# Kernel tuning notes

Measured on AMD Instinct MI355X. Metric: run time of the kernel, lower is better.

Reference implementation:

```python
import jax, jax.numpy as jnp
import numpy as np
import math

ATTN_C = 32
HEADS = 8
IN_C = 256
PAIR_C = 128
B, M, N = 1, 128, 256


def _layernorm(x, w, b, eps=1e-5):
    mu = jnp.mean(x, axis=-1, keepdims=True)
    xc = x - mu
    var = jnp.mean(xc * xc, axis=-1, keepdims=True)
    return xc * jax.lax.rsqrt(var + eps) * w + b


def setup_inputs() -> dict:
    key = jax.random.key(0)
    ks = jax.random.split(key, 10)
    s1 = 1.0 / math.sqrt(IN_C)
    s2 = 1.0 / math.sqrt(PAIR_C)
    s3 = 1.0 / math.sqrt(ATTN_C * HEADS)
    return {
        "x1d": jax.random.normal(ks[0], (B, M, N, IN_C), jnp.float32),
        "x2d": jax.random.normal(ks[1], (B, N, N, PAIR_C), jnp.float32),
        "norm_w": jnp.ones((IN_C,), jnp.float32),
        "norm_b": jnp.zeros((IN_C,), jnp.float32),
        "qkv_w": jax.random.normal(ks[2], (3 * ATTN_C * HEADS, IN_C), jnp.float32) * s1,
        "x2d_w": jax.random.normal(ks[3], (HEADS, PAIR_C), jnp.float32) * s2,
        "gate_w": jax.random.normal(ks[4], (ATTN_C * HEADS, IN_C), jnp.float32) * s1,
        "gate_b": jnp.zeros((ATTN_C * HEADS,), jnp.float32),
        "final_w": jax.random.normal(ks[5], (IN_C, ATTN_C * HEADS), jnp.float32) * s3,
        "final_b": jnp.zeros((IN_C,), jnp.float32),
    }


def reference(x1d, x2d, norm_w, norm_b, qkv_w, x2d_w, gate_w, gate_b, final_w, final_b):
    c, h = ATTN_C, HEADS
    x = _layernorm(x1d, norm_w, norm_b)                      # [B,M,N,IN_C]
    qkv = (x @ qkv_w.T).reshape(*x.shape[:-1], c, 3 * h)     # [B,M,N,c,3h]
    q, k, v = qkv[..., :h], qkv[..., h:2 * h], qkv[..., 2 * h:]
    aff = jnp.einsum('bmich,bmjch->bmijh', q, k)             # [B,M,N,N,H]
    gate = jax.nn.sigmoid(x @ gate_w.T + gate_b).reshape(*x.shape[:-1], c, h)
    factor = 1.0 / math.sqrt(c)
    bias = (x2d @ x2d_w.T) * factor                          # [B,N,N,H]
    weights = jax.nn.softmax(aff + bias[:, None], axis=-2)   # softmax over j
    out = jnp.einsum('bmrch,bmirh->bmich', v, weights) * gate
    out = out.reshape(*x.shape[:-1], c * h) @ final_w.T + final_b
    return out
```

## Files before the change

### kernel.cpp

```cpp
#include <hip/hip_runtime.h>
#include <math.h>

typedef short bf16x8 __attribute__((ext_vector_type(8)));
typedef float f32x4  __attribute__((ext_vector_type(4)));

#define NPOS 32768

#define OFF_CHI   0u
#define OFF_AHI   100663296u
#define OFF_ATTN  134217728u
#define OFF_BIAST 150994944u
#define OFF_WHI   153354240u
#define OFF_W2P   154402816u
#define OFF_GBP   154533888u

__device__ __forceinline__ short f2bf(float x) {
    unsigned int u = __float_as_uint(x);
    unsigned int r = (u + 0x7FFFu + ((u >> 16) & 1u)) >> 16;
    return (short)r;
}
__device__ __forceinline__ float bf2f(short s) {
    return __uint_as_float(((unsigned int)(unsigned short)s) << 16);
}
__device__ __forceinline__ void async_copy16(const void* g, void* l) {
    __builtin_amdgcn_global_load_lds(
        (const __attribute__((address_space(1))) unsigned int*)g,
        (__attribute__((address_space(3))) unsigned int*)l, 16, 0, 0);
}

#define PREP_LN   8192
#define PREP_CW   9473
__global__ __launch_bounds__(256) void k_prep(
    const float* __restrict__ x, const float* __restrict__ nw, const float* __restrict__ nb,
    const float* __restrict__ qkvw, const float* __restrict__ gatew,
    const float* __restrict__ gateb, const float* __restrict__ finalw,
    const float* __restrict__ x2d, const float* __restrict__ x2dw,
    short* __restrict__ Ahi, short* __restrict__ Whi, short* __restrict__ W2p,
    float* __restrict__ gbp, float* __restrict__ biasT) {
    __shared__ float xs[64][132];
    __shared__ float ws[8][132];
    const int bid = blockIdx.x;
    const int t = threadIdx.x;

    if (bid < PREP_LN) {
        int wid = (bid * 256 + t) >> 6;
        int lane = t & 63;
        const float4 v = ((const float4*)(x + (size_t)wid * 256))[lane];
        float s  = v.x + v.y + v.z + v.w;
        float ss = v.x*v.x + v.y*v.y + v.z*v.z + v.w*v.w;
        #pragma unroll
        for (int o = 32; o; o >>= 1) {
            s  += __shfl_xor(s,  o, 64);
            ss += __shfl_xor(ss, o, 64);
        }
        float mu  = s * (1.0f / 256);
        float var = ss * (1.0f / 256) - mu * mu;
        float rs  = rsqrtf(var + 1e-5f);
        const float4 wv = ((const float4*)nw)[lane];
        const float4 bv = ((const float4*)nb)[lane];
        float y[4] = {(v.x - mu) * rs * wv.x + bv.x, (v.y - mu) * rs * wv.y + bv.y,
                      (v.z - mu) * rs * wv.z + bv.z, (v.w - mu) * rs * wv.w + bv.w};
        short h4[4];
        #pragma unroll
        for (int i = 0; i < 4; ++i) h4[i] = f2bf(y[i]);
        *(short4*)(Ahi + (size_t)wid * 256 + lane * 4) = *(short4*)h4;
    } else if (bid < PREP_CW) {
        int r = bid - PREP_LN;
        if (r < 1024) {
            int which = r >> 8, h = (r >> 5) & 7, c = r & 31;
            const float* src = (which < 3) ? qkvw + (size_t)(c * 24 + which * 8 + h) * 256
                                           : gatew + (size_t)(c * 8 + h) * 256;
            Whi[(size_t)r * 256 + t] = f2bf(src[t]);
        } else if (r < 1280) {
            int o = r - 1024;
            int h = t >> 5, c = t & 31;
            W2p[(size_t)o * 256 + t] = f2bf(finalw[(size_t)o * 256 + c * 8 + h]);
        } else {
            int h = t >> 5, c = t & 31;
            gbp[t] = gateb[c * 8 + h];
        }
    } else {
        const int wid0 = (bid - PREP_CW) * 64;
        #pragma unroll
        for (int r = 0; r < 8; ++r) {
            int g = r * 256 + t;
            int row = g >> 5, c4 = g & 31;
            float4 v = *(const float4*)(x2d + (size_t)(wid0 + row) * 128 + c4 * 4);
            *(float4*)&xs[row][c4 * 4] = v;
        }
        {
            int h = t >> 5, c4 = t & 31;
            *(float4*)&ws[h][c4 * 4] = *(const float4*)(x2dw + h * 128 + c4 * 4);
        }
        __syncthreads();
        const float f = 0.17677669529663687f;
        const int i = wid0 >> 8;
        #pragma unroll
        for (int kk = 0; kk < 2; ++kk) {
            int o = t + kk * 256;
            int row = o >> 3, h = o & 7;
            float acc = 0.f;
            #pragma unroll
            for (int c4 = 0; c4 < 32; ++c4) {
                float4 xv = *(const float4*)&xs[row][c4 * 4];
                float4 wv = *(const float4*)&ws[h][c4 * 4];
                acc += xv.x * wv.x + xv.y * wv.y + xv.z * wv.z + xv.w * wv.w;
            }
            int j = (wid0 & 255) + row;
            biasT[(((h * 256 + j)) << 8) + i] = acc * f;
        }
    }
}

__global__ __launch_bounds__(256, 2) void k_gemm1m(
    const short* __restrict__ Ahi, const short* __restrict__ Whi,
    const float* __restrict__ gbp, short* __restrict__ Chi) {
    __shared__ short As[256 * 64];
    __shared__ short Bs[128 * 64];
    const int t = threadIdx.x;
    const int wave = t >> 6, lane = t & 63, ln15 = lane & 15, quad = lane >> 4;
    const int posBase = blockIdx.x * 256;
    const int nb = blockIdx.y;

    f32x4 acc[4][8];
    #pragma unroll
    for (int a = 0; a < 4; ++a)
        #pragma unroll
        for (int b = 0; b < 8; ++b) acc[a][b] = (f32x4){0.f, 0.f, 0.f, 0.f};

    for (int k0 = 0; k0 < 256; k0 += 64) {
        #pragma unroll
        for (int r = 0; r < 8; ++r) {
            int g = r * 256 + t;
            int row = g >> 3, cs = g & 7;
            int colg = cs ^ (row & 7);
            async_copy16(Ahi + (size_t)(posBase + row) * 256 + k0 + colg * 8, &As[g * 8]);
        }
        #pragma unroll
        for (int r = 0; r < 4; ++r) {
            int g = r * 256 + t;
            int row = g >> 3, cs = g & 7;
            int colg = cs ^ (row & 7);
            async_copy16(Whi + (size_t)(nb * 128 + row) * 256 + k0 + colg * 8, &Bs[g * 8]);
        }
        __syncthreads();
        #pragma unroll
        for (int kc = 0; kc < 2; ++kc) {
            bf16x8 af[4], bfr[8];
            #pragma unroll
            for (int it = 0; it < 4; ++it) {
                int rowa = wave * 64 + it * 16 + ln15;
                int c8a = (kc * 4 + quad) ^ (rowa & 7);
                af[it] = *(const bf16x8*)&As[rowa * 64 + c8a * 8];
            }
            #pragma unroll
            for (int nt = 0; nt < 8; ++nt) {
                int rowb = nt * 16 + ln15;
                int c8b = (kc * 4 + quad) ^ (rowb & 7);
                bfr[nt] = *(const bf16x8*)&Bs[rowb * 64 + c8b * 8];
            }
            #pragma unroll
            for (int it = 0; it < 4; ++it)
                #pragma unroll
                for (int nt = 0; nt < 8; ++nt)
                    acc[it][nt] = __builtin_amdgcn_mfma_f32_16x16x32_bf16(
                        bfr[nt], af[it], acc[it][nt], 0, 0, 0);
        }
        __syncthreads();
    }
    const bool isgate = (nb >= 6);
    #pragma unroll
    for (int it = 0; it < 4; ++it) {
        size_t pos = posBase + wave * 64 + it * 16 + ln15;
        #pragma unroll
        for (int nt = 0; nt < 8; ++nt) {
            int ncol0 = nb * 128 + nt * 16 + quad * 4;
            float v[4];
            #pragma unroll
            for (int r = 0; r < 4; ++r) v[r] = acc[it][nt][r];
            if (isgate) {
                const float4 gb = *(const float4*)&gbp[ncol0 - 768];
                v[0] = 1.0f / (1.0f + __expf(-(v[0] + gb.x)));
                v[1] = 1.0f / (1.0f + __expf(-(v[1] + gb.y)));
                v[2] = 1.0f / (1.0f + __expf(-(v[2] + gb.z)));
                v[3] = 1.0f / (1.0f + __expf(-(v[3] + gb.w)));
            }
            unsigned w0 = (unsigned)(unsigned short)f2bf(v[0])
                        | ((unsigned)(unsigned short)f2bf(v[1]) << 16);
            unsigned w1 = (unsigned)(unsigned short)f2bf(v[2])
                        | ((unsigned)(unsigned short)f2bf(v[3]) << 16);
            *(uint2*)&Chi[pos * 1024 + ncol0] = make_uint2(w0, w1);
        }
    }
}

__global__ __launch_bounds__(512) void k_attn3(
    const short* __restrict__ Chi, const float* __restrict__ biasT,
    short* __restrict__ attnB) {
    __shared__ short Khi[256 * 32];
    __shared__ short VT[32 * 264];
    __shared__ short Pl[8][16][40];

    const int mh = blockIdx.x;
    const int m = mh >> 3, h = mh & 7;
    const int t = threadIdx.x;
    const int wave = t >> 6, lane = t & 63, ln15 = lane & 15, quad = lane >> 4;
    const int i0 = wave * 32;

    #pragma unroll
    for (int r = 0; r < 2; ++r) {
        int g = r * 512 + t;
        int j = g >> 2, c16 = g & 3;
        int cs = c16 ^ (j & 3);
        const short* gp = Chi + (size_t)(m * 256 + j) * 1024 + 256 + h * 32 + cs * 8;
        async_copy16(gp, &Khi[(r * 512 + wave * 64) * 8]);
    }
    {
        int j = t & 255, c0 = (t >> 8) * 16;
        const short* vp = Chi + (size_t)(m * 256 + j) * 1024 + 512 + h * 32 + c0;
        bf16x8 v0 = *(const bf16x8*)vp;
        bf16x8 v1 = *(const bf16x8*)(vp + 8);
        #pragma unroll
        for (int c = 0; c < 8; ++c) VT[(c0 + c) * 264 + j] = v0[c];
        #pragma unroll
        for (int c = 0; c < 8; ++c) VT[(c0 + 8 + c) * 264 + j] = v1[c];
    }
    bf16x8 qhi[2];
    #pragma unroll
    for (int it = 0; it < 2; ++it) {
        int i = i0 + it * 16 + ln15;
        qhi[it] = *(const bf16x8*)(Chi + (size_t)(m * 256 + i) * 1024 + h * 32 + quad * 8);
    }
    __syncthreads();

    float lacc[2] = {0.f, 0.f};
    f32x4 Oacc[2][2];
    #pragma unroll
    for (int a = 0; a < 2; ++a) {
        Oacc[a][0] = (f32x4){0.f, 0.f, 0.f, 0.f};
        Oacc[a][1] = (f32x4){0.f, 0.f, 0.f, 0.f};
    }
    const float* bp = biasT + (size_t)h * 65536;

    for (int j0 = 0; j0 < 256; j0 += 32) {
        bf16x8 kfh[2], vf[2];
        #pragma unroll
        for (int jt = 0; jt < 2; ++jt) {
            int j = j0 + jt * 16 + ln15;
            int cs = quad ^ (j & 3);
            kfh[jt] = *(const bf16x8*)&Khi[j * 32 + cs * 8];
        }
        #pragma unroll
        for (int ct = 0; ct < 2; ++ct) {
            int c = ct * 16 + ln15;
            vf[ct] = *(const bf16x8*)&VT[c * 264 + j0 + quad * 8];
        }
        #pragma unroll
        for (int it = 0; it < 2; ++it) {
            int i = i0 + it * 16 + ln15;
            float b0[4], b1[4];
            #pragma unroll
            for (int r = 0; r < 4; ++r) {
                b0[r] = bp[(j0 + quad * 4 + r) * 256 + i];
                b1[r] = bp[(j0 + 16 + quad * 4 + r) * 256 + i];
            }
            f32x4 s0 = (f32x4){0.f, 0.f, 0.f, 0.f};
            f32x4 s1 = (f32x4){0.f, 0.f, 0.f, 0.f};
            s0 = __builtin_amdgcn_mfma_f32_16x16x32_bf16(kfh[0], qhi[it], s0, 0, 0, 0);
            s1 = __builtin_amdgcn_mfma_f32_16x16x32_bf16(kfh[1], qhi[it], s1, 0, 0, 0);
            float p[8], ps = 0.f;
            #pragma unroll
            for (int r = 0; r < 4; ++r) { p[r] = __expf(s0[r] + b0[r]); ps += p[r]; }
            #pragma unroll
            for (int r = 0; r < 4; ++r) { p[4 + r] = __expf(s1[r] + b1[r]); ps += p[4 + r]; }
            lacc[it] += ps;
            unsigned long long pw0 =
                  (unsigned long long)(unsigned short)f2bf(p[0])
                | ((unsigned long long)(unsigned short)f2bf(p[1]) << 16)
                | ((unsigned long long)(unsigned short)f2bf(p[2]) << 32)
                | ((unsigned long long)(unsigned short)f2bf(p[3]) << 48);
            unsigned long long pw1 =
                  (unsigned long long)(unsigned short)f2bf(p[4])
                | ((unsigned long long)(unsigned short)f2bf(p[5]) << 16)
                | ((unsigned long long)(unsigned short)f2bf(p[6]) << 32)
                | ((unsigned long long)(unsigned short)f2bf(p[7]) << 48);
            *(unsigned long long*)&Pl[wave][ln15][quad * 4]      = pw0;
            *(unsigned long long*)&Pl[wave][ln15][16 + quad * 4] = pw1;
            bf16x8 pf = *(const bf16x8*)&Pl[wave][ln15][quad * 8];
            Oacc[it][0] = __builtin_amdgcn_mfma_f32_16x16x32_bf16(pf, vf[0], Oacc[it][0], 0, 0, 0);
            Oacc[it][1] = __builtin_amdgcn_mfma_f32_16x16x32_bf16(pf, vf[1], Oacc[it][1], 0, 0, 0);
        }
    }
    #pragma unroll
    for (int it = 0; it < 2; ++it) {
        float l = lacc[it];
        l += __shfl_xor(l, 16, 64);
        l += __shfl_xor(l, 32, 64);
        float inv = 1.0f / l;
        float invr[4];
        #pragma unroll
        for (int r = 0; r < 4; ++r) invr[r] = __shfl(inv, quad * 4 + r, 16);
        #pragma unroll
        for (int ct = 0; ct < 2; ++ct) {
            int c = ct * 16 + ln15;
            #pragma unroll
            for (int r = 0; r < 4; ++r) {
                int i = i0 + it * 16 + quad * 4 + r;
                float g = bf2f(Chi[(size_t)(m * 256 + i) * 1024 + 768 + h * 32 + c]);
                float val = Oacc[it][ct][r] * invr[r] * g;
                attnB[(size_t)(m * 256 + i) * 256 + h * 32 + c] = f2bf(val);
            }
        }
    }
}

__global__ __launch_bounds__(256) void k_gemm2m(
    const short* __restrict__ A, const short* __restrict__ W2p,
    const float* __restrict__ fb, float* __restrict__ out) {
    __shared__ short As[128 * 64];
    __shared__ short Bs[128 * 64];
    const int t = threadIdx.x;
    const int wave = t >> 6, lane = t & 63, ln15 = lane & 15, quad = lane >> 4;
    const int posBase = blockIdx.x * 128;
    const int nb = blockIdx.y;
    const int i0w = (wave & 1) * 64, n0w = (wave >> 1) * 64;

    f32x4 acc[4][4];
    #pragma unroll
    for (int a = 0; a < 4; ++a)
        #pragma unroll
        for (int b = 0; b < 4; ++b) acc[a][b] = (f32x4){0.f, 0.f, 0.f, 0.f};

    for (int k0 = 0; k0 < 256; k0 += 64) {
        #pragma unroll
        for (int r = 0; r < 4; ++r) {
            int g = r * 256 + t;
            int row = g >> 3, cs = g & 7;
            int colg = cs ^ (row & 7);
            const short* ga = A + (size_t)(posBase + row) * 256 + k0 + colg * 8;
            async_copy16(ga, &As[(r * 256 + wave * 64) * 8]);
            const short* gb = W2p + (size_t)(nb * 128 + row) * 256 + k0 + colg * 8;
            async_copy16(gb, &Bs[(r * 256 + wave * 64) * 8]);
        }
        __syncthreads();
        #pragma unroll
        for (int kc = 0; kc < 2; ++kc) {
            bf16x8 af[4], bfr[4];
            #pragma unroll
            for (int it = 0; it < 4; ++it) {
                int rowa = i0w + it * 16 + ln15;
                int c8a = (kc * 4 + quad) ^ (rowa & 7);
                af[it] = *(const bf16x8*)&As[rowa * 64 + c8a * 8];
                int rowb = n0w + it * 16 + ln15;
                int c8b = (kc * 4 + quad) ^ (rowb & 7);
                bfr[it] = *(const bf16x8*)&Bs[rowb * 64 + c8b * 8];
            }
            #pragma unroll
            for (int it = 0; it < 4; ++it)
                #pragma unroll
                for (int nt = 0; nt < 4; ++nt)
                    acc[it][nt] = __builtin_amdgcn_mfma_f32_16x16x32_bf16(
                        bfr[nt], af[it], acc[it][nt], 0, 0, 0);
        }
        __syncthreads();
    }
    #pragma unroll
    for (int it = 0; it < 4; ++it) {
        size_t pos = posBase + i0w + it * 16 + ln15;
        #pragma unroll
        for (int nt = 0; nt < 4; ++nt) {
            int ncol0 = nb * 128 + n0w + nt * 16 + quad * 4;
            const float4 fbv = *(const float4*)&fb[ncol0];
            float4 o;
            o.x = acc[it][nt][0] + fbv.x;
            o.y = acc[it][nt][1] + fbv.y;
            o.z = acc[it][nt][2] + fbv.z;
            o.w = acc[it][nt][3] + fbv.w;
            *(float4*)&out[pos * 256 + ncol0] = o;
        }
    }
}

extern "C" void kernel_launch(void* const* d_in, const int* in_sizes, int n_in,
                              void* d_out, int out_size, void* d_ws, size_t ws_size,
                              hipStream_t stream) {
    const float* x1d     = (const float*)d_in[0];
    const float* x2d     = (const float*)d_in[1];
    const float* norm_w  = (const float*)d_in[2];
    const float* norm_b  = (const float*)d_in[3];
    const float* qkv_w   = (const float*)d_in[4];
    const float* x2d_w   = (const float*)d_in[5];
    const float* gate_w  = (const float*)d_in[6];
    const float* gate_b  = (const float*)d_in[7];
    const float* final_w = (const float*)d_in[8];
    const float* final_b = (const float*)d_in[9];
    float* out = (float*)d_out;
    char* w = (char*)d_ws;

    short* Chi   = (short*)(w + OFF_CHI);
    short* Ahi   = (short*)(w + OFF_AHI);
    short* attnB = (short*)(w + OFF_ATTN);
    float* biasT = (float*)(w + OFF_BIAST);
    short* Whi   = (short*)(w + OFF_WHI);
    short* W2p   = (short*)(w + OFF_W2P);
    float* gbp   = (float*)(w + OFF_GBP);

    k_prep<<<10497, 256, 0, stream>>>(x1d, norm_w, norm_b, qkv_w, gate_w, gate_b,
                                      final_w, x2d, x2d_w, Ahi, Whi, W2p, gbp, biasT);
    k_gemm1m<<<dim3(128, 8), 256, 0, stream>>>(Ahi, Whi, gbp, Chi);
    k_attn3<<<1024, 512, 0, stream>>>(Chi, biasT, attnB);
    k_gemm2m<<<dim3(256, 2), 256, 0, stream>>>(attnB, W2p, final_b, out);
}
```

Baseline: 227.5 us.

## Double-buffer gemm1 LDS tiles and shrink block tile to 128x128

Restructures the first projection GEMM to use a 128x128 block tile with a 2x2 wave grid, and double-buffers the A and B LDS tiles. The next K-slice's async copies are issued before computing the current one, gated by explicit vmcnt waits and raw s_barrier calls. This is meant to hide global-load latency behind MFMA work and to double the grid size for better CU fill. In exchange each wave holds fewer accumulators, and the explicit waitcnt/barrier sequencing is fragile.

```diff
diff --git a/kernel.cpp b/kernel.cpp
--- a/kernel.cpp
+++ b/kernel.cpp
@@ -112,69 +112,80 @@
     }
 }
 
-__global__ __launch_bounds__(256, 2) void k_gemm1m(
+__global__ __launch_bounds__(256) void k_gemm1m(
     const short* __restrict__ Ahi, const short* __restrict__ Whi,
     const float* __restrict__ gbp, short* __restrict__ Chi) {
-    __shared__ short As[256 * 64];
-    __shared__ short Bs[128 * 64];
+    __shared__ short As[2][128 * 64];
+    __shared__ short Bs[2][128 * 64];
     const int t = threadIdx.x;
     const int wave = t >> 6, lane = t & 63, ln15 = lane & 15, quad = lane >> 4;
-    const int posBase = blockIdx.x * 256;
+    const int posBase = blockIdx.x * 128;
     const int nb = blockIdx.y;
-
-    f32x4 acc[4][8];
+    const int i0w = (wave & 1) * 64, n0w = (wave >> 1) * 64;
+
+    f32x4 acc[4][4];
     #pragma unroll
     for (int a = 0; a < 4; ++a)
         #pragma unroll
-        for (int b = 0; b < 8; ++b) acc[a][b] = (f32x4){0.f, 0.f, 0.f, 0.f};
-
-    for (int k0 = 0; k0 < 256; k0 += 64) {
-        #pragma unroll
-        for (int r = 0; r < 8; ++r) {
-            int g = r * 256 + t;
-            int row = g >> 3, cs = g & 7;
-            int colg = cs ^ (row & 7);
-            async_copy16(Ahi + (size_t)(posBase + row) * 256 + k0 + colg * 8, &As[g * 8]);
-        }
+        for (int b = 0; b < 4; ++b) acc[a][b] = (f32x4){0.f, 0.f, 0.f, 0.f};
+
+    auto stage = [&](int buf, int k0) {
         #pragma unroll
         for (int r = 0; r < 4; ++r) {
             int g = r * 256 + t;
             int row = g >> 3, cs = g & 7;
             int colg = cs ^ (row & 7);
-            async_copy16(Whi + (size_t)(nb * 128 + row) * 256 + k0 + colg * 8, &Bs[g * 8]);
-        }
-        __syncthreads();
+            size_t aoff = (size_t)(posBase + row) * 256 + k0 + colg * 8;
+            size_t boff = (size_t)(nb * 128 + row) * 256 + k0 + colg * 8;
+            int ldst = (r * 256 + wave * 64) * 8;
+            async_copy16(Ahi + aoff, &As[buf][ldst]);
+            async_copy16(Whi + boff, &Bs[buf][ldst]);
+        }
+    };
+
+    stage(0, 0);
+    #pragma unroll
+    for (int ks = 0; ks < 4; ++ks) {
+        const int cur = ks & 1;
+        if (ks < 3) {
+            stage(cur ^ 1, (ks + 1) * 64);
+            asm volatile("s_waitcnt vmcnt(8)" ::: "memory");
+        } else {
+            asm volatile("s_waitcnt vmcnt(0)" ::: "memory");
+        }
+        __builtin_amdgcn_sched_barrier(0);
+        __builtin_amdgcn_s_barrier();
+        __builtin_amdgcn_sched_barrier(0);
         #pragma unroll
         for (int kc = 0; kc < 2; ++kc) {
-            bf16x8 af[4], bfr[8];
+            bf16x8 af[4], bfr[4];
             #pragma unroll
             for (int it = 0; it < 4; ++it) {
-                int rowa = wave * 64 + it * 16 + ln15;
+                int rowa = i0w + it * 16 + ln15;
                 int c8a = (kc * 4 + quad) ^ (rowa & 7);
-                af[it] = *(const bf16x8*)&As[rowa * 64 + c8a * 8];
-            }
-            #pragma unroll
-            for (int nt = 0; nt < 8; ++nt) {
-                int rowb = nt * 16 + ln15;
+                af[it] = *(const bf16x8*)&As[cur][rowa * 64 + c8a * 8];
+                int rowb = n0w + it * 16 + ln15;
                 int c8b = (kc * 4 + quad) ^ (rowb & 7);
-                bfr[nt] = *(const bf16x8*)&Bs[rowb * 64 + c8b * 8];
+                bfr[it] = *(const bf16x8*)&Bs[cur][rowb * 64 + c8b * 8];
             }
             #pragma unroll
             for (int it = 0; it < 4; ++it)
                 #pragma unroll
-                for (int nt = 0; nt < 8; ++nt)
+                for (int nt = 0; nt < 4; ++nt)
                     acc[it][nt] = __builtin_amdgcn_mfma_f32_16x16x32_bf16(
                         bfr[nt], af[it], acc[it][nt], 0, 0, 0);
         }
-        __syncthreads();
+        __builtin_amdgcn_sched_barrier(0);
+        __builtin_amdgcn_s_barrier();
+        __builtin_amdgcn_sched_barrier(0);
     }
     const bool isgate = (nb >= 6);
     #pragma unroll
     for (int it = 0; it < 4; ++it) {
-        size_t pos = posBase + wave * 64 + it * 16 + ln15;
-        #pragma unroll
-        for (int nt = 0; nt < 8; ++nt) {
-            int ncol0 = nb * 128 + nt * 16 + quad * 4;
+        size_t pos = posBase + i0w + it * 16 + ln15;
+        #pragma unroll
+        for (int nt = 0; nt < 4; ++nt) {
+            int ncol0 = nb * 128 + n0w + nt * 16 + quad * 4;
             float v[4];
             #pragma unroll
             for (int r = 0; r < 4; ++r) v[r] = acc[it][nt][r];
@@ -407,7 +418,7 @@
 
     k_prep<<<10497, 256, 0, stream>>>(x1d, norm_w, norm_b, qkv_w, gate_w, gate_b,
                                       final_w, x2d, x2d_w, Ahi, Whi, W2p, gbp, biasT);
-    k_gemm1m<<<dim3(128, 8), 256, 0, stream>>>(Ahi, Whi, gbp, Chi);
+    k_gemm1m<<<dim3(256, 8), 256, 0, stream>>>(Ahi, Whi, gbp, Chi);
     k_attn3<<<1024, 512, 0, stream>>>(Chi, biasT, attnB);
     k_gemm2m<<<dim3(256, 2), 256, 0, stream>>>(attnB, W2p, final_b, out);
 }
```

After: 224.6 us. No clear change (-1.2%).

## Fuse QKV/gate projection GEMM into attention kernel per (m, head) block

Applied to the files above, without the earlier changes.

Merges the projection GEMM and the attention kernel: each block computes Q, K, V and gate for its row m and head h directly into shared memory, then runs attention from LDS. This removes the large Chi intermediate (a 64 MB bf16 write and reread) and one launch. In exchange, the A tile for each m is reloaded once per head (8x redundant A reads), and the per-block GEMM tile is smaller. Shared memory is reused across the two phases, and launch bounds of 512 threads with 4 blocks per CU constrain registers.

```diff
diff --git a/kernel.cpp b/kernel.cpp
--- a/kernel.cpp
+++ b/kernel.cpp
@@ -6,7 +6,6 @@
 
 #define NPOS 32768
 
-#define OFF_CHI   0u
 #define OFF_AHI   100663296u
 #define OFF_ATTN  134217728u
 #define OFF_BIAST 150994944u
@@ -112,44 +111,54 @@
     }
 }
 
-__global__ __launch_bounds__(256, 2) void k_gemm1m(
+__global__ __launch_bounds__(512, 4) void k_fused(
     const short* __restrict__ Ahi, const short* __restrict__ Whi,
-    const float* __restrict__ gbp, short* __restrict__ Chi) {
-    __shared__ short As[256 * 64];
-    __shared__ short Bs[128 * 64];
+    const float* __restrict__ gbp, const float* __restrict__ biasT,
+    short* __restrict__ attnB) {
+    __shared__ __align__(16) short smem[38144];
+    short* As  = smem;
+    short* Ws  = smem + 16384;
+    short* Khi = smem;
+    short* VT  = smem + 8192;
+    short* Qs  = smem + 16640;
+    short* Gs  = smem + 24832;
+    short* Pl  = smem + 33024;
+
+    const int mh = blockIdx.x;
+    const int h = mh >> 7, m = mh & 127;
     const int t = threadIdx.x;
     const int wave = t >> 6, lane = t & 63, ln15 = lane & 15, quad = lane >> 4;
-    const int posBase = blockIdx.x * 256;
-    const int nb = blockIdx.y;
-
-    f32x4 acc[4][8];
-    #pragma unroll
-    for (int a = 0; a < 4; ++a)
+    const int i0 = wave * 32;
+
+    f32x4 acc[2][8];
+    #pragma unroll
+    for (int a = 0; a < 2; ++a)
         #pragma unroll
         for (int b = 0; b < 8; ++b) acc[a][b] = (f32x4){0.f, 0.f, 0.f, 0.f};
 
     for (int k0 = 0; k0 < 256; k0 += 64) {
         #pragma unroll
-        for (int r = 0; r < 8; ++r) {
-            int g = r * 256 + t;
+        for (int r = 0; r < 4; ++r) {
+            int g = r * 512 + t;
             int row = g >> 3, cs = g & 7;
             int colg = cs ^ (row & 7);
-            async_copy16(Ahi + (size_t)(posBase + row) * 256 + k0 + colg * 8, &As[g * 8]);
-        }
-        #pragma unroll
-        for (int r = 0; r < 4; ++r) {
-            int g = r * 256 + t;
+            async_copy16(Ahi + (size_t)(m * 256 + row) * 256 + k0 + colg * 8, &As[g * 8]);
+        }
+        #pragma unroll
+        for (int r = 0; r < 2; ++r) {
+            int g = r * 512 + t;
             int row = g >> 3, cs = g & 7;
             int colg = cs ^ (row & 7);
-            async_copy16(Whi + (size_t)(nb * 128 + row) * 256 + k0 + colg * 8, &Bs[g * 8]);
+            int nrow = (row >> 5) * 256 + h * 32 + (row & 31);
+            async_copy16(Whi + (size_t)nrow * 256 + k0 + colg * 8, &Ws[g * 8]);
         }
         __syncthreads();
         #pragma unroll
         for (int kc = 0; kc < 2; ++kc) {
-            bf16x8 af[4], bfr[8];
-            #pragma unroll
-            for (int it = 0; it < 4; ++it) {
-                int rowa = wave * 64 + it * 16 + ln15;
+            bf16x8 af[2], bfr[8];
+            #pragma unroll
+            for (int it = 0; it < 2; ++it) {
+                int rowa = i0 + it * 16 + ln15;
                 int c8a = (kc * 4 + quad) ^ (rowa & 7);
                 af[it] = *(const bf16x8*)&As[rowa * 64 + c8a * 8];
             }
@@ -157,10 +166,10 @@
             for (int nt = 0; nt < 8; ++nt) {
                 int rowb = nt * 16 + ln15;
                 int c8b = (kc * 4 + quad) ^ (rowb & 7);
-                bfr[nt] = *(const bf16x8*)&Bs[rowb * 64 + c8b * 8];
-            }
-            #pragma unroll
-            for (int it = 0; it < 4; ++it)
+                bfr[nt] = *(const bf16x8*)&Ws[rowb * 64 + c8b * 8];
+            }
+            #pragma unroll
+            for (int it = 0; it < 2; ++it)
                 #pragma unroll
                 for (int nt = 0; nt < 8; ++nt)
                     acc[it][nt] = __builtin_amdgcn_mfma_f32_16x16x32_bf16(
@@ -168,71 +177,49 @@
         }
         __syncthreads();
     }
-    const bool isgate = (nb >= 6);
-    #pragma unroll
-    for (int it = 0; it < 4; ++it) {
-        size_t pos = posBase + wave * 64 + it * 16 + ln15;
+
+    #pragma unroll
+    for (int it = 0; it < 2; ++it) {
+        int j = i0 + it * 16 + ln15;
+        int sw = j & 3;
         #pragma unroll
         for (int nt = 0; nt < 8; ++nt) {
-            int ncol0 = nb * 128 + nt * 16 + quad * 4;
-            float v[4];
-            #pragma unroll
-            for (int r = 0; r < 4; ++r) v[r] = acc[it][nt][r];
-            if (isgate) {
-                const float4 gb = *(const float4*)&gbp[ncol0 - 768];
-                v[0] = 1.0f / (1.0f + __expf(-(v[0] + gb.x)));
-                v[1] = 1.0f / (1.0f + __expf(-(v[1] + gb.y)));
-                v[2] = 1.0f / (1.0f + __expf(-(v[2] + gb.z)));
-                v[3] = 1.0f / (1.0f + __expf(-(v[3] + gb.w)));
-            }
-            unsigned w0 = (unsigned)(unsigned short)f2bf(v[0])
-                        | ((unsigned)(unsigned short)f2bf(v[1]) << 16);
-            unsigned w1 = (unsigned)(unsigned short)f2bf(v[2])
-                        | ((unsigned)(unsigned short)f2bf(v[3]) << 16);
-            *(uint2*)&Chi[pos * 1024 + ncol0] = make_uint2(w0, w1);
-        }
-    }
-}
-
-__global__ __launch_bounds__(512) void k_attn3(
-    const short* __restrict__ Chi, const float* __restrict__ biasT,
-    short* __restrict__ attnB) {
-    __shared__ short Khi[256 * 32];
-    __shared__ short VT[32 * 264];
-    __shared__ short Pl[8][16][40];
-
-    const int mh = blockIdx.x;
-    const int m = mh >> 3, h = mh & 7;
-    const int t = threadIdx.x;
-    const int wave = t >> 6, lane = t & 63, ln15 = lane & 15, quad = lane >> 4;
-    const int i0 = wave * 32;
-
-    #pragma unroll
-    for (int r = 0; r < 2; ++r) {
-        int g = r * 512 + t;
-        int j = g >> 2, c16 = g & 3;
-        int cs = c16 ^ (j & 3);
-        const short* gp = Chi + (size_t)(m * 256 + j) * 1024 + 256 + h * 32 + cs * 8;
-        async_copy16(gp, &Khi[(r * 512 + wave * 64) * 8]);
-    }
-    {
-        int j = t & 255, c0 = (t >> 8) * 16;
-        const short* vp = Chi + (size_t)(m * 256 + j) * 1024 + 512 + h * 32 + c0;
-        bf16x8 v0 = *(const bf16x8*)vp;
-        bf16x8 v1 = *(const bf16x8*)(vp + 8);
-        #pragma unroll
-        for (int c = 0; c < 8; ++c) VT[(c0 + c) * 264 + j] = v0[c];
-        #pragma unroll
-        for (int c = 0; c < 8; ++c) VT[(c0 + 8 + c) * 264 + j] = v1[c];
-    }
+            int which = nt >> 1;
+            int cloc0 = (nt & 1) * 16 + quad * 4;
+            float v0 = acc[it][nt][0], v1 = acc[it][nt][1];
+            float v2 = acc[it][nt][2], v3 = acc[it][nt][3];
+            if (which == 3) {
+                const float4 gb = *(const float4*)&gbp[h * 32 + cloc0];
+                v0 = 1.0f / (1.0f + __expf(-(v0 + gb.x)));
+                v1 = 1.0f / (1.0f + __expf(-(v1 + gb.y)));
+                v2 = 1.0f / (1.0f + __expf(-(v2 + gb.z)));
+                v3 = 1.0f / (1.0f + __expf(-(v3 + gb.w)));
+            }
+            short s0 = f2bf(v0), s1 = f2bf(v1), s2 = f2bf(v2), s3 = f2bf(v3);
+            if (which == 2) {
+                VT[(cloc0 + 0) * 264 + j] = s0;
+                VT[(cloc0 + 1) * 264 + j] = s1;
+                VT[(cloc0 + 2) * 264 + j] = s2;
+                VT[(cloc0 + 3) * 264 + j] = s3;
+            } else {
+                unsigned w0 = (unsigned)(unsigned short)s0 | ((unsigned)(unsigned short)s1 << 16);
+                unsigned w1 = (unsigned)(unsigned short)s2 | ((unsigned)(unsigned short)s3 << 16);
+                int cg = cloc0 >> 3, off = cloc0 & 7;
+                short* dst = (which == 0) ? &Qs[j * 32 + (cg ^ sw) * 8 + off]
+                           : (which == 1) ? &Khi[j * 32 + (cg ^ sw) * 8 + off]
+                                          : &Gs[j * 32 + cloc0];
+                *(uint2*)dst = make_uint2(w0, w1);
+            }
+        }
+    }
+    __syncthreads();
+
     bf16x8 qhi[2];
     #pragma unroll
     for (int it = 0; it < 2; ++it) {
         int i = i0 + it * 16 + ln15;
-        qhi[it] = *(const bf16x8*)(Chi + (size_t)(m * 256 + i) * 1024 + h * 32 + quad * 8);
-    }
-    __syncthreads();
-
+        qhi[it] = *(const bf16x8*)&Qs[i * 32 + ((quad ^ (i & 3))) * 8];
+    }
     float lacc[2] = {0.f, 0.f};
     f32x4 Oacc[2][2];
     #pragma unroll
@@ -284,9 +271,10 @@
                 | ((unsigned long long)(unsigned short)f2bf(p[5]) << 16)
                 | ((unsigned long long)(unsigned short)f2bf(p[6]) << 32)
                 | ((unsigned long long)(unsigned short)f2bf(p[7]) << 48);
-            *(unsigned long long*)&Pl[wave][ln15][quad * 4]      = pw0;
-            *(unsigned long long*)&Pl[wave][ln15][16 + quad * 4] = pw1;
-            bf16x8 pf = *(const bf16x8*)&Pl[wave][ln15][quad * 8];
+            short* plp = &Pl[(wave * 16 + ln15) * 40];
+            *(unsigned long long*)&plp[quad * 4]      = pw0;
+            *(unsigned long long*)&plp[16 + quad * 4] = pw1;
+            bf16x8 pf = *(const bf16x8*)&plp[quad * 8];
             Oacc[it][0] = __builtin_amdgcn_mfma_f32_16x16x32_bf16(pf, vf[0], Oacc[it][0], 0, 0, 0);
             Oacc[it][1] = __builtin_amdgcn_mfma_f32_16x16x32_bf16(pf, vf[1], Oacc[it][1], 0, 0, 0);
         }
@@ -306,7 +294,7 @@
             #pragma unroll
             for (int r = 0; r < 4; ++r) {
                 int i = i0 + it * 16 + quad * 4 + r;
-                float g = bf2f(Chi[(size_t)(m * 256 + i) * 1024 + 768 + h * 32 + c]);
+                float g = bf2f(Gs[i * 32 + c]);
                 float val = Oacc[it][ct][r] * invr[r] * g;
                 attnB[(size_t)(m * 256 + i) * 256 + h * 32 + c] = f2bf(val);
             }
@@ -397,7 +385,6 @@
     float* out = (float*)d_out;
     char* w = (char*)d_ws;
 
-    short* Chi   = (short*)(w + OFF_CHI);
     short* Ahi   = (short*)(w + OFF_AHI);
     short* attnB = (short*)(w + OFF_ATTN);
     float* biasT = (float*)(w + OFF_BIAST);
@@ -407,7 +394,6 @@
 
     k_prep<<<10497, 256, 0, stream>>>(x1d, norm_w, norm_b, qkv_w, gate_w, gate_b,
                                       final_w, x2d, x2d_w, Ahi, Whi, W2p, gbp, biasT);
-    k_gemm1m<<<dim3(128, 8), 256, 0, stream>>>(Ahi, Whi, gbp, Chi);
-    k_attn3<<<1024, 512, 0, stream>>>(Chi, biasT, attnB);
+    k_fused<<<1024, 512, 0, stream>>>(Ahi, Whi, gbp, biasT, attnB);
     k_gemm2m<<<dim3(256, 2), 256, 0, stream>>>(attnB, W2p, final_b, out);
 }
```

Result: faster. 193.0 us (-15.2%).
